# Kernel tuning notes

Hardware: AMD Instinct MI355X
Metric: run time of the kernel (lower is better)

The kernel has to match this reference:

```python
import jax, jax.numpy as jnp
import numpy as np

BATCH, SEQ, IN_DIM, UNITS = 64, 512, 512, 1024

def _glorot(key, shape):
    fan_in, fan_out = shape
    lim = jnp.sqrt(6.0 / (fan_in + fan_out))
    return jax.random.uniform(key, shape, jnp.float32, -lim, lim)

def setup_inputs() -> dict:
    key = jax.random.key(0)
    ks = jax.random.split(key, 6)
    x = jax.random.normal(ks[0], (BATCH, SEQ, IN_DIM), dtype=jnp.float32)
    d = IN_DIM + UNITS
    W_f = _glorot(ks[1], (d, UNITS))
    W_i = _glorot(ks[2], (d, UNITS))
    W_o = _glorot(ks[3], (d, UNITS))
    W_c = _glorot(ks[4], (d, UNITS))
    b_f = jnp.ones((UNITS,), jnp.float32)  # unit_forget_bias=True
    b_i = jnp.zeros((UNITS,), jnp.float32)
    b_o = jnp.zeros((UNITS,), jnp.float32)
    b_c = jnp.zeros((UNITS,), jnp.float32)
    return {"x": x, "W_f": W_f, "W_i": W_i, "W_o": W_o, "W_c": W_c,
            "b_f": b_f, "b_i": b_i, "b_o": b_o, "b_c": b_c}

def reference(x, W_f, W_i, W_o, W_c, b_f, b_i, b_o, b_c):
    B = x.shape[0]
    h0 = jnp.zeros((B, UNITS), x.dtype)
    c0 = jnp.zeros((B, UNITS), x.dtype)

    def step(carry, x_t):
        h, c = carry
        xh = jnp.concatenate([x_t, h], axis=1)  # [B, IN_DIM+UNITS]
        f = jax.nn.sigmoid(xh @ W_f + b_f)
        i = jax.nn.sigmoid(xh @ W_i + b_i)
        c_cand = jnp.tanh(xh @ W_c + b_c)
        c_new = f * c + i * c_cand
        o = jax.nn.sigmoid(xh @ W_o + b_o)
        h_new = o * jnp.tanh(c_new)
        return (h_new, c_new), h_new

    x_tbf = jnp.swapaxes(x, 0, 1)  # [SEQ, B, IN_DIM]
    _, hs = jax.lax.scan(step, (h0, c0), x_tbf)
    return jnp.swapaxes(hs, 0, 1)  # [B, SEQ, UNITS]
```

## Files before the change

### kernel.cpp

```cpp
#include <hip/hip_runtime.h>
#include <hip/hip_bf16.h>

typedef __attribute__((ext_vector_type(8))) _Float16 half8;
typedef __attribute__((ext_vector_type(4))) _Float16 half4v;
typedef __attribute__((ext_vector_type(4))) float f32x4;
typedef __attribute__((ext_vector_type(2))) float f32x2;
typedef unsigned long long u64;

#define T_SEQ 512
#define N_B   64
#define D_IN  512
#define N_U   1024

#define OFF_CNT   0ull
#define OFF_HSEQ  65536ull
#define OFF_XB    (OFF_HSEQ + 513ull*131072ull)
#define OFF_WBT   (OFF_XB + 33554432ull)
#define OFF_WHT   (OFF_WBT + 4194304ull)
#define OFF_BIAS  (OFF_WHT + 8388608ull)
#define OFF_FSEQ  (OFF_BIAS + 16384ull)

__device__ __forceinline__ float sigf(float x) { return 1.f / (1.f + __expf(-x)); }
__device__ __forceinline__ float tanhfast(float x) { return 2.f / (1.f + __expf(-2.f * x)) - 1.f; }

__global__ __launch_bounds__(256) void pack_x(const float* __restrict__ x, _Float16* __restrict__ xb) {
  size_t i4 = ((size_t)blockIdx.x * 256 + threadIdx.x) * 4;
  int m = (int)(i4 >> 9), k = (int)(i4 & 511);
  int t = m >> 6, b = m & 63;
  const float4 v = *(const float4*)(x + ((size_t)b * T_SEQ + t) * D_IN + k);
  half4v o; o.x = (_Float16)v.x; o.y = (_Float16)v.y; o.z = (_Float16)v.z; o.w = (_Float16)v.w;
  *(half4v*)(xb + i4) = o;
}

__global__ __launch_bounds__(256) void pack_w(const float* __restrict__ Wf, const float* __restrict__ Wi,
                                              const float* __restrict__ Wo, const float* __restrict__ Wc,
                                              _Float16* __restrict__ WbT, _Float16* __restrict__ WhT) {
  size_t i4 = ((size_t)blockIdx.x * 256 + threadIdx.x) * 4;
  int n = (int)(i4 / 1536), k = (int)(i4 % 1536);
  int g = n & 3, u = n >> 2;
  const float* W = (g == 0) ? Wf : (g == 1) ? Wi : (g == 2) ? Wo : Wc;
  half4v o;
  o.x = (_Float16)W[(size_t)(k + 0) * N_U + u];
  o.y = (_Float16)W[(size_t)(k + 1) * N_U + u];
  o.z = (_Float16)W[(size_t)(k + 2) * N_U + u];
  o.w = (_Float16)W[(size_t)(k + 3) * N_U + u];
  if (k < D_IN) *(half4v*)(WbT + (size_t)n * D_IN + k) = o;
  else          *(half4v*)(WhT + (size_t)n * N_U + (k - D_IN)) = o;
}

__global__ __launch_bounds__(256) void pack_b(const float* __restrict__ bf_, const float* __restrict__ bi_,
                                              const float* __restrict__ bo_, const float* __restrict__ bc_,
                                              float* __restrict__ biasv) {
  int n = blockIdx.x * 256 + threadIdx.x;
  int g = n & 3, u = n >> 2;
  biasv[n] = (g == 0) ? bf_[u] : (g == 1) ? bi_[u] : (g == 2) ? bo_[u] : bc_[u];
}

__device__ __forceinline__ void quadtr(f32x4 v, int gg, float& F, float& I, float& O, float& G) {
  const bool o1 = gg & 1, o2 = gg & 2;
  float s01 = o1 ? v[0] : v[1];
  float s23 = o1 ? v[2] : v[3];
  float r01 = __int_as_float(__builtin_amdgcn_ds_swizzle(__float_as_int(s01), 0x041F));
  float r23 = __int_as_float(__builtin_amdgcn_ds_swizzle(__float_as_int(s23), 0x041F));
  float x0 = o1 ? r01 : v[0];
  float x1 = o1 ? v[1] : r01;
  float x2 = o1 ? r23 : v[2];
  float x3 = o1 ? v[3] : r23;
  float s02 = o2 ? x0 : x2;
  float s13 = o2 ? x1 : x3;
  float r02 = __int_as_float(__builtin_amdgcn_ds_swizzle(__float_as_int(s02), 0x081F));
  float r13 = __int_as_float(__builtin_amdgcn_ds_swizzle(__float_as_int(s13), 0x081F));
  F = o2 ? r02 : x0;
  I = o2 ? r13 : x1;
  O = o2 ? x2 : r02;
  G = o2 ? x3 : r13;
}

__global__ __launch_bounds__(256, 1) void lstm_rec(
    const _Float16* __restrict__ xb, const _Float16* __restrict__ WbT,
    const _Float16* __restrict__ WhT, const float* __restrict__ biasv,
    _Float16* __restrict__ hseq, float* __restrict__ out, unsigned* __restrict__ fseq) {
  const int wg = blockIdx.x;
  const int tid = threadIdx.x;
  const int l = tid & 63, w = tid >> 6;
  const int lr = l & 15, lkb = (l >> 4) * 8;
  const int arow = w * 16 + lr;
  const int uu = lr >> 2, gg = l & 3;
  const int u0 = wg * 8 + 2 * uu;
  const int R  = w * 16 + (l >> 4) * 4 + gg;

  __shared__ half8 wlds[96 * 64];

  for (int idx = tid; idx < 96 * 64; idx += 256) {
    int s = idx >> 6, l2 = idx & 63;
    int kk = s >> 1, nf = s & 1;
    int uu2 = (l2 & 15) >> 2, gg2 = l2 & 3, lkb2 = (l2 >> 4) * 8;
    int col = (wg * 8 + 2 * uu2 + nf) * 4 + gg2;
    const _Float16* src = (kk < 16)
      ? WbT + (size_t)col * D_IN + kk * 32 + lkb2
      : WhT + (size_t)col * N_U + (kk - 16) * 32 + lkb2;
    wlds[idx] = *(const half8*)src;
  }

  const float bv0 = biasv[(size_t)u0 * 4 + gg];
  const float bv1 = biasv[(size_t)(u0 + 1) * 4 + gg];
  float c0 = 0.f, c1 = 0.f;

  __syncthreads();

  half8 wh0[16], wh1[16];
#pragma unroll
  for (int j = 0; j < 16; j++) {
    wh0[j] = wlds[((16 + j) * 2 + 0) * 64 + l];
    wh1[j] = wlds[((16 + j) * 2 + 1) * 64 + l];
  }

  half8 xfn[16];
  {
    const _Float16* xa = xb + (size_t)arow * D_IN + lkb;
#pragma unroll
    for (int j = 0; j < 16; j++) xfn[j] = *(const half8*)(xa + j * 32);
  }
  f32x4 a0 = {bv0, bv0, bv0, bv0};
  f32x4 a1 = {bv1, bv1, bv1, bv1};
#pragma unroll
  for (int j = 0; j < 16; j++) {
    a0 = __builtin_amdgcn_mfma_f32_16x16x32_f16(xfn[j], wlds[(j * 2 + 0) * 64 + l], a0, 0, 0, 0);
    a1 = __builtin_amdgcn_mfma_f32_16x16x32_f16(xfn[j], wlds[(j * 2 + 1) * 64 + l], a1, 0, 0, 0);
  }

  for (int g = 0; g < T_SEQ; g++) {
    if (g > 0) {
      unsigned* fg = fseq + (size_t)g * 128;
      if (tid < 128) {
        unsigned v = *((volatile const unsigned*)fg + tid);
        if (v == 0u) {
          while (__hip_atomic_load(&fg[tid], __ATOMIC_RELAXED, __HIP_MEMORY_SCOPE_AGENT) == 0u)
            __builtin_amdgcn_s_sleep(1);
        }
      }
      asm volatile("" ::: "memory");
      __syncthreads();
    }

    const _Float16* hp = hseq + (size_t)g * (N_B * N_U) + (size_t)arow * N_U + lkb;
    half8 hf[32];
#pragma unroll
    for (int j = 0; j < 32; j++) hf[j] = *(const half8*)(hp + j * 32);

    const int gn = (g + 1 < T_SEQ) ? g + 1 : 0;
    const _Float16* xa = xb + ((size_t)gn * N_B + arow) * D_IN + lkb;
#pragma unroll
    for (int j = 0; j < 16; j++) xfn[j] = *(const half8*)(xa + j * 32);

    f32x4 b0 = {0.f, 0.f, 0.f, 0.f};
    f32x4 b1 = {0.f, 0.f, 0.f, 0.f};
#pragma unroll
    for (int j = 0; j < 16; j++) {
      a0 = __builtin_amdgcn_mfma_f32_16x16x32_f16(hf[j],      wh0[j], a0, 0, 0, 0);
      a1 = __builtin_amdgcn_mfma_f32_16x16x32_f16(hf[j],      wh1[j], a1, 0, 0, 0);
      b0 = __builtin_amdgcn_mfma_f32_16x16x32_f16(hf[j + 16], wlds[((32 + j) * 2 + 0) * 64 + l], b0, 0, 0, 0);
      b1 = __builtin_amdgcn_mfma_f32_16x16x32_f16(hf[j + 16], wlds[((32 + j) * 2 + 1) * 64 + l], b1, 0, 0, 0);
    }
    a0 += b0;
    a1 += b1;

    float F0, I0, O0, G0, F1, I1, O1, G1;
    quadtr(a0, gg, F0, I0, O0, G0);
    quadtr(a1, gg, F1, I1, O1, G1);
    c0 = sigf(F0) * c0 + sigf(I0) * tanhfast(G0);
    c1 = sigf(F1) * c1 + sigf(I1) * tanhfast(G1);
    float h0v = sigf(O0) * tanhfast(c0);
    float h1v = sigf(O1) * tanhfast(c1);

    unsigned hw;
    { union { _Float16 h[2]; unsigned u; } pk; pk.h[0] = (_Float16)h0v; pk.h[1] = (_Float16)h1v; hw = pk.u; }
    unsigned* hn = (unsigned*)(hseq + (size_t)(g + 1) * (N_B * N_U) + (size_t)R * N_U + u0);
    (void)__hip_atomic_exchange(hn, hw, __ATOMIC_RELAXED, __HIP_MEMORY_SCOPE_AGENT);

    a0 = f32x4{bv0, bv0, bv0, bv0};
    a1 = f32x4{bv1, bv1, bv1, bv1};
#pragma unroll
    for (int j = 0; j < 8; j++) {
      a0 = __builtin_amdgcn_mfma_f32_16x16x32_f16(xfn[j], wlds[(j * 2 + 0) * 64 + l], a0, 0, 0, 0);
      a1 = __builtin_amdgcn_mfma_f32_16x16x32_f16(xfn[j], wlds[(j * 2 + 1) * 64 + l], a1, 0, 0, 0);
    }

    __syncthreads();
    if (tid == 0)
      (void)__hip_atomic_exchange(&fseq[(size_t)(g + 1) * 128 + wg], 1u, __ATOMIC_RELAXED, __HIP_MEMORY_SCOPE_AGENT);

#pragma unroll
    for (int j = 8; j < 16; j++) {
      a0 = __builtin_amdgcn_mfma_f32_16x16x32_f16(xfn[j], wlds[(j * 2 + 0) * 64 + l], a0, 0, 0, 0);
      a1 = __builtin_amdgcn_mfma_f32_16x16x32_f16(xfn[j], wlds[(j * 2 + 1) * 64 + l], a1, 0, 0, 0);
    }

    f32x2 ov; ov.x = h0v; ov.y = h1v;
    __builtin_nontemporal_store(ov, (f32x2*)(out + ((size_t)R * T_SEQ + g) * N_U + u0));
  }
}

extern "C" void kernel_launch(void* const* d_in, const int* in_sizes, int n_in,
                              void* d_out, int out_size, void* d_ws, size_t ws_size,
                              hipStream_t stream) {
  const float* x  = (const float*)d_in[0];
  const float* Wf = (const float*)d_in[1];
  const float* Wi = (const float*)d_in[2];
  const float* Wo = (const float*)d_in[3];
  const float* Wc = (const float*)d_in[4];
  const float* bf_ = (const float*)d_in[5];
  const float* bi_ = (const float*)d_in[6];
  const float* bo_ = (const float*)d_in[7];
  const float* bc_ = (const float*)d_in[8];
  float* out = (float*)d_out;

  char* ws = (char*)d_ws;
  _Float16* hseq = (_Float16*)(ws + OFF_HSEQ);
  _Float16* xb   = (_Float16*)(ws + OFF_XB);
  _Float16* WbT  = (_Float16*)(ws + OFF_WBT);
  _Float16* WhT  = (_Float16*)(ws + OFF_WHT);
  float* biasv = (float*)(ws + OFF_BIAS);
  unsigned* fseq = (unsigned*)(ws + OFF_FSEQ);

  (void)hipMemsetAsync(d_ws, 0, 1 << 20, stream);
  (void)hipMemsetAsync(ws + OFF_FSEQ, 0, 513 * 512, stream);
  pack_x<<<16384, 256, 0, stream>>>(x, xb);
  pack_w<<<6144, 256, 0, stream>>>(Wf, Wi, Wo, Wc, WbT, WhT);
  pack_b<<<16, 256, 0, stream>>>(bf_, bi_, bo_, bc_, biasv);

  lstm_rec<<<128, 256, 0, stream>>>(xb, WbT, WhT, biasv, hseq, out, fseq);
}
```

Baseline: 3.140 ms.

## Split recurrent LSTM across 256 workgroups with four units each

The persistent recurrent kernel now launches 256 workgroups instead of 128, and each one owns 4 hidden units (16 gate columns) instead of 8. This halves the per-step MFMA chain, the LDS weight footprint and the register-resident recurrent weights per workgroup. The goal is a shorter critical path per timestep on a part with enough compute units to hold all workgroups at once. In exchange, the per-step grid barrier now polls 256 flags. Hidden-state writes pair neighbouring units through a lane swizzle so they stay 32-bit atomics, while output stores become scalar floats.

```diff
diff --git a/kernel.cpp b/kernel.cpp
--- a/kernel.cpp
+++ b/kernel.cpp
@@ -86,34 +86,29 @@
   const int lr = l & 15, lkb = (l >> 4) * 8;
   const int arow = w * 16 + lr;
   const int uu = lr >> 2, gg = l & 3;
-  const int u0 = wg * 8 + 2 * uu;
+  const int ug = wg * 4 + uu;
   const int R  = w * 16 + (l >> 4) * 4 + gg;
 
-  __shared__ half8 wlds[96 * 64];
-
-  for (int idx = tid; idx < 96 * 64; idx += 256) {
-    int s = idx >> 6, l2 = idx & 63;
-    int kk = s >> 1, nf = s & 1;
-    int uu2 = (l2 & 15) >> 2, gg2 = l2 & 3, lkb2 = (l2 >> 4) * 8;
-    int col = (wg * 8 + 2 * uu2 + nf) * 4 + gg2;
+  __shared__ half8 wlds[48 * 64];
+
+  for (int idx = tid; idx < 48 * 64; idx += 256) {
+    int kk = idx >> 6, l2 = idx & 63;
+    int lr2 = l2 & 15, lkb2 = (l2 >> 4) * 8;
+    int col = wg * 16 + lr2;
     const _Float16* src = (kk < 16)
       ? WbT + (size_t)col * D_IN + kk * 32 + lkb2
       : WhT + (size_t)col * N_U + (kk - 16) * 32 + lkb2;
     wlds[idx] = *(const half8*)src;
   }
 
-  const float bv0 = biasv[(size_t)u0 * 4 + gg];
-  const float bv1 = biasv[(size_t)(u0 + 1) * 4 + gg];
-  float c0 = 0.f, c1 = 0.f;
+  const float bv0 = biasv[(size_t)wg * 16 + lr];
+  float c0 = 0.f;
 
   __syncthreads();
 
-  half8 wh0[16], wh1[16];
-#pragma unroll
-  for (int j = 0; j < 16; j++) {
-    wh0[j] = wlds[((16 + j) * 2 + 0) * 64 + l];
-    wh1[j] = wlds[((16 + j) * 2 + 1) * 64 + l];
-  }
+  half8 wh0[16];
+#pragma unroll
+  for (int j = 0; j < 16; j++) wh0[j] = wlds[(16 + j) * 64 + l];
 
   half8 xfn[16];
   {
@@ -122,17 +117,14 @@
     for (int j = 0; j < 16; j++) xfn[j] = *(const half8*)(xa + j * 32);
   }
   f32x4 a0 = {bv0, bv0, bv0, bv0};
-  f32x4 a1 = {bv1, bv1, bv1, bv1};
-#pragma unroll
-  for (int j = 0; j < 16; j++) {
-    a0 = __builtin_amdgcn_mfma_f32_16x16x32_f16(xfn[j], wlds[(j * 2 + 0) * 64 + l], a0, 0, 0, 0);
-    a1 = __builtin_amdgcn_mfma_f32_16x16x32_f16(xfn[j], wlds[(j * 2 + 1) * 64 + l], a1, 0, 0, 0);
-  }
+#pragma unroll
+  for (int j = 0; j < 16; j++)
+    a0 = __builtin_amdgcn_mfma_f32_16x16x32_f16(xfn[j], wlds[j * 64 + l], a0, 0, 0, 0);
 
   for (int g = 0; g < T_SEQ; g++) {
     if (g > 0) {
-      unsigned* fg = fseq + (size_t)g * 128;
-      if (tid < 128) {
+      unsigned* fg = fseq + (size_t)g * 256;
+      {
         unsigned v = *((volatile const unsigned*)fg + tid);
         if (v == 0u) {
           while (__hip_atomic_load(&fg[tid], __ATOMIC_RELAXED, __HIP_MEMORY_SCOPE_AGENT) == 0u)
@@ -154,50 +146,41 @@
     for (int j = 0; j < 16; j++) xfn[j] = *(const half8*)(xa + j * 32);
 
     f32x4 b0 = {0.f, 0.f, 0.f, 0.f};
-    f32x4 b1 = {0.f, 0.f, 0.f, 0.f};
 #pragma unroll
     for (int j = 0; j < 16; j++) {
-      a0 = __builtin_amdgcn_mfma_f32_16x16x32_f16(hf[j],      wh0[j], a0, 0, 0, 0);
-      a1 = __builtin_amdgcn_mfma_f32_16x16x32_f16(hf[j],      wh1[j], a1, 0, 0, 0);
-      b0 = __builtin_amdgcn_mfma_f32_16x16x32_f16(hf[j + 16], wlds[((32 + j) * 2 + 0) * 64 + l], b0, 0, 0, 0);
-      b1 = __builtin_amdgcn_mfma_f32_16x16x32_f16(hf[j + 16], wlds[((32 + j) * 2 + 1) * 64 + l], b1, 0, 0, 0);
+      a0 = __builtin_amdgcn_mfma_f32_16x16x32_f16(hf[j],      wh0[j],                a0, 0, 0, 0);
+      b0 = __builtin_amdgcn_mfma_f32_16x16x32_f16(hf[j + 16], wlds[(32 + j) * 64 + l], b0, 0, 0, 0);
     }
     a0 += b0;
-    a1 += b1;
-
-    float F0, I0, O0, G0, F1, I1, O1, G1;
+
+    float F0, I0, O0, G0;
     quadtr(a0, gg, F0, I0, O0, G0);
-    quadtr(a1, gg, F1, I1, O1, G1);
     c0 = sigf(F0) * c0 + sigf(I0) * tanhfast(G0);
-    c1 = sigf(F1) * c1 + sigf(I1) * tanhfast(G1);
     float h0v = sigf(O0) * tanhfast(c0);
-    float h1v = sigf(O1) * tanhfast(c1);
-
-    unsigned hw;
-    { union { _Float16 h[2]; unsigned u; } pk; pk.h[0] = (_Float16)h0v; pk.h[1] = (_Float16)h1v; hw = pk.u; }
-    unsigned* hn = (unsigned*)(hseq + (size_t)(g + 1) * (N_B * N_U) + (size_t)R * N_U + u0);
-    (void)__hip_atomic_exchange(hn, hw, __ATOMIC_RELAXED, __HIP_MEMORY_SCOPE_AGENT);
+
+    unsigned hs;
+    { union { _Float16 h; unsigned short s; } pk; pk.h = (_Float16)h0v; hs = (unsigned)pk.s; }
+    unsigned pw = (unsigned)__builtin_amdgcn_ds_swizzle((int)hs, 0x101F);
+    if ((l & 4) == 0) {
+      unsigned payload = hs | (pw << 16);
+      unsigned* hn = (unsigned*)(hseq + (size_t)(g + 1) * (N_B * N_U) + (size_t)R * N_U + ug);
+      (void)__hip_atomic_exchange(hn, payload, __ATOMIC_RELAXED, __HIP_MEMORY_SCOPE_AGENT);
+    }
 
     a0 = f32x4{bv0, bv0, bv0, bv0};
-    a1 = f32x4{bv1, bv1, bv1, bv1};
-#pragma unroll
-    for (int j = 0; j < 8; j++) {
-      a0 = __builtin_amdgcn_mfma_f32_16x16x32_f16(xfn[j], wlds[(j * 2 + 0) * 64 + l], a0, 0, 0, 0);
-      a1 = __builtin_amdgcn_mfma_f32_16x16x32_f16(xfn[j], wlds[(j * 2 + 1) * 64 + l], a1, 0, 0, 0);
-    }
+#pragma unroll
+    for (int j = 0; j < 8; j++)
+      a0 = __builtin_amdgcn_mfma_f32_16x16x32_f16(xfn[j], wlds[j * 64 + l], a0, 0, 0, 0);
 
     __syncthreads();
     if (tid == 0)
-      (void)__hip_atomic_exchange(&fseq[(size_t)(g + 1) * 128 + wg], 1u, __ATOMIC_RELAXED, __HIP_MEMORY_SCOPE_AGENT);
-
-#pragma unroll
-    for (int j = 8; j < 16; j++) {
-      a0 = __builtin_amdgcn_mfma_f32_16x16x32_f16(xfn[j], wlds[(j * 2 + 0) * 64 + l], a0, 0, 0, 0);
-      a1 = __builtin_amdgcn_mfma_f32_16x16x32_f16(xfn[j], wlds[(j * 2 + 1) * 64 + l], a1, 0, 0, 0);
-    }
-
-    f32x2 ov; ov.x = h0v; ov.y = h1v;
-    __builtin_nontemporal_store(ov, (f32x2*)(out + ((size_t)R * T_SEQ + g) * N_U + u0));
+      (void)__hip_atomic_exchange(&fseq[(size_t)(g + 1) * 256 + wg], 1u, __ATOMIC_RELAXED, __HIP_MEMORY_SCOPE_AGENT);
+
+#pragma unroll
+    for (int j = 8; j < 16; j++)
+      a0 = __builtin_amdgcn_mfma_f32_16x16x32_f16(xfn[j], wlds[j * 64 + l], a0, 0, 0, 0);
+
+    __builtin_nontemporal_store(h0v, out + ((size_t)R * T_SEQ + g) * N_U + ug);
   }
 }
 
@@ -224,10 +207,10 @@
   unsigned* fseq = (unsigned*)(ws + OFF_FSEQ);
 
   (void)hipMemsetAsync(d_ws, 0, 1 << 20, stream);
-  (void)hipMemsetAsync(ws + OFF_FSEQ, 0, 513 * 512, stream);
+  (void)hipMemsetAsync(ws + OFF_FSEQ, 0, 513 * 1024, stream);
   pack_x<<<16384, 256, 0, stream>>>(x, xb);
   pack_w<<<6144, 256, 0, stream>>>(Wf, Wi, Wo, Wc, WbT, WhT);
   pack_b<<<16, 256, 0, stream>>>(bf_, bi_, bo_, bc_, biasv);
 
-  lstm_rec<<<128, 256, 0, stream>>>(xb, WbT, WhT, biasv, hseq, out, fseq);
-}
+  lstm_rec<<<256, 256, 0, stream>>>(xb, WbT, WhT, biasv, hseq, out, fseq);
+}
```

Result: slower. 3.254 ms (+3.6%).
